# Kernel optimization log

Measured on AMD Instinct MI355X. Metric: run time of the kernel, lower is better.

The kernel has to match this reference:

```python
import jax, jax.numpy as jnp
import numpy as np

B, D, C = 4096, 4096, 1024


def setup_inputs() -> dict:
    key = jax.random.key(0)
    kx, kw = jax.random.split(key)
    x = jax.random.normal(kx, (B, D), dtype=jnp.float32)
    # kaiming_normal_ with nonlinearity='relu': std = sqrt(2 / fan_in)
    W = jax.random.normal(kw, (C, D), dtype=jnp.float32) * jnp.sqrt(2.0 / D)
    return {"x": x, "W": W}


def reference(x, W):
    # Original: -( (x[:, :, None] - W.T[None, :, :])**2 ).mean(axis=1)
    d = x.shape[1]
    x_sq = jnp.sum(x * x, axis=1, keepdims=True)        # [B, 1]
    w_sq = jnp.sum(W * W, axis=1)[None, :]              # [1, C]
    cross = jnp.einsum('bd,cd->bc', x, W)               # [B, C] tensor-core GEMM
    return -(x_sq - 2.0 * cross + w_sq) / d
```

## Files before the change

### kernel.cpp

```cpp
#include <hip/hip_runtime.h>
#include <hip/hip_bf16.h>


typedef float f32x4 __attribute__((ext_vector_type(4)));
typedef float f32x2 __attribute__((ext_vector_type(2)));
typedef float f32x16 __attribute__((ext_vector_type(16)));
typedef int i32x4 __attribute__((ext_vector_type(4)));
typedef int i32x8 __attribute__((ext_vector_type(8)));

#define BDIM 4096
#define DDIM 4096
#define CDIM 1024
#define TM 128
#define TN 128
#define BK 64
#define KSPLIT 4
#define NIT ((DDIM / KSPLIT) / BK)
#define SCALE 32.0f
#define INV_SS (1.0f/1024.0f)
#define PSCALE 0.0625f

#define SYNC_LGKM() asm volatile("s_waitcnt lgkmcnt(0)\n\ts_barrier" ::: "memory")

__global__ __launch_bounds__(256) void cvt_rowsq(
    const float* __restrict__ x, const float* __restrict__ W,
    unsigned char* __restrict__ xb, unsigned char* __restrict__ wb,
    float* __restrict__ xsq, float* __restrict__ wsq)
{
    const int lane = threadIdx.x & 63;
    const int row = blockIdx.x * 4 + (threadIdx.x >> 6);

    const float* src;
    unsigned char* dst;
    float* sq;
    if (row < BDIM) {
        src = x + (size_t)row * DDIM;
        dst = xb + (size_t)row * DDIM;
        sq = xsq + row;
    } else {
        int r = row - BDIM;
        src = W + (size_t)r * DDIM;
        dst = wb + (size_t)r * DDIM;
        sq = wsq + r;
    }

    const float4* s4 = (const float4*)src;
    unsigned int* d4 = (unsigned int*)dst;
    float a = 0.f;
    #pragma unroll
    for (int s = 0; s < DDIM / 4 / 64; ++s) {
        float4 f = s4[lane + 64 * s];
        a += f.x * f.x + f.y * f.y + f.z * f.z + f.w * f.w;
        unsigned int p = 0;
        p = __builtin_amdgcn_cvt_pk_fp8_f32(f.x * SCALE, f.y * SCALE, p, false);
        p = __builtin_amdgcn_cvt_pk_fp8_f32(f.z * SCALE, f.w * SCALE, p, true);
        d4[lane + 64 * s] = p;
    }
    #pragma unroll
    for (int off = 32; off > 0; off >>= 1) a += __shfl_down(a, off);
    if (lane == 0) *sq = a;
}

struct Pref { i32x4 a0, a1, b0, b1; };

__device__ __forceinline__ i32x8 rd8(const unsigned char* p0,
                                     const unsigned char* p1) {
    i32x4 lo = *(const i32x4*)p0;
    i32x4 hi = *(const i32x4*)p1;
    return __builtin_shufflevector(lo, hi, 0, 1, 2, 3, 4, 5, 6, 7);
}

#define MXMFMA(A, Bv, C)                                                  \
    __builtin_amdgcn_mfma_scale_f32_32x32x64_f8f6f4(                      \
        (A), (Bv), (C), 0, 0, 0, 0x7F7F7F7F, 0, 0x7F7F7F7F)

__global__ __launch_bounds__(256, 3) void gemm_eucl(
    const unsigned char* __restrict__ xb,
    const unsigned char* __restrict__ wb,
    unsigned int* __restrict__ part)
{
    __shared__ unsigned char sm[2 * 16384];

    const int tid = threadIdx.x;
    const int lane = tid & 63;
    const int wid = tid >> 6;
    const int bm = blockIdx.x * TM;
    const int bn = blockIdx.y * TN;
    const int ks = blockIdx.z * (DDIM / KSPLIT);
    const int wm = (wid >> 1) * 64;
    const int wn = (wid & 1) * 64;

    const int r0 = tid >> 2, c = tid & 3;
    const unsigned int oA0 = (unsigned int)((bm + r0) * DDIM + ks + c * 16);
    const unsigned int oA1 = oA0 + 64u * DDIM;
    const unsigned int oB0 = (unsigned int)((bn + r0) * DDIM + ks + c * 16);
    const unsigned int oB1 = oB0 + 64u * DDIM;

    const int wo0 = r0 * 64 + ((c ^ ((r0 >> 1) & 3)) * 16);

    const int sswz = (lane >> 1) & 3;
    const int c0 = (lane >> 5) * 2;
    const int m0 = wm + (lane & 31);
    const int n0 = wn + (lane & 31);
    const int aof0 = m0 * 64 + ((c0 ^ sswz) * 16);
    const int aof1 = m0 * 64 + (((c0 + 1) ^ sswz) * 16);
    const int bof0 = n0 * 64 + ((c0 ^ sswz) * 16);
    const int bof1 = n0 * 64 + (((c0 + 1) ^ sswz) * 16);

    f32x16 acc[4] = {};

#define LOADSET(S, KT)                                                   \
    do {                                                                 \
        (S).a0 = *(const i32x4*)(xb + oA0 + (KT) * BK);                  \
        (S).a1 = *(const i32x4*)(xb + oA1 + (KT) * BK);                  \
        (S).b0 = *(const i32x4*)(wb + oB0 + (KT) * BK);                  \
        (S).b1 = *(const i32x4*)(wb + oB1 + (KT) * BK);                  \
    } while (0)

#define WRITESET(buf, S)                                                 \
    do {                                                                 \
        unsigned char* sA = sm + (buf) * 16384;                          \
        unsigned char* sB = sA + 8192;                                   \
        *(i32x4*)(sA + wo0) = (S).a0;                                    \
        *(i32x4*)(sA + wo0 + 4096) = (S).a1;                             \
        *(i32x4*)(sB + wo0) = (S).b0;                                    \
        *(i32x4*)(sB + wo0 + 4096) = (S).b1;                             \
    } while (0)

#define COMPUTE(buf)                                                     \
    do {                                                                 \
        const unsigned char* sA = sm + (buf) * 16384;                    \
        const unsigned char* sB = sA + 8192;                             \
        i32x8 fb0 = rd8(sB + bof0, sB + bof1);                           \
        i32x8 fb1 = rd8(sB + bof0 + 2048, sB + bof1 + 2048);             \
        i32x8 fa0 = rd8(sA + aof0, sA + aof1);                           \
        acc[0] = MXMFMA(fa0, fb0, acc[0]);                               \
        i32x8 fa1 = rd8(sA + aof0 + 2048, sA + aof1 + 2048);             \
        acc[1] = MXMFMA(fa0, fb1, acc[1]);                               \
        acc[2] = MXMFMA(fa1, fb0, acc[2]);                               \
        acc[3] = MXMFMA(fa1, fb1, acc[3]);                               \
    } while (0)

    Pref S[3];
    LOADSET(S[0], 0);
    LOADSET(S[1], 1);
    LOADSET(S[2], 2);
    WRITESET(0, S[0]);
    SYNC_LGKM();

    #pragma unroll
    for (int k = 0; k < NIT - 1; ++k) {
        if (k < NIT - 3) LOADSET(S[k % 3], k + 3);
        COMPUTE(k & 1);
        WRITESET((k + 1) & 1, S[(k + 1) % 3]);
        SYNC_LGKM();
    }
    COMPUTE((NIT - 1) & 1);

    unsigned int* p = part
        + (((size_t)blockIdx.z * 256 + (blockIdx.x * 8 + blockIdx.y)) * 16) * 256;
    #pragma unroll
    for (int t = 0; t < 4; ++t)
        #pragma unroll
        for (int g = 0; g < 4; ++g) {
            unsigned int pk = 0;
            pk = __builtin_amdgcn_cvt_pk_fp8_f32(
                acc[t][g * 4 + 0] * PSCALE, acc[t][g * 4 + 1] * PSCALE, pk, false);
            pk = __builtin_amdgcn_cvt_pk_fp8_f32(
                acc[t][g * 4 + 2] * PSCALE, acc[t][g * 4 + 3] * PSCALE, pk, true);
            p[(t * 4 + g) * 256 + tid] = pk;
        }
#undef LOADSET
#undef WRITESET
#undef COMPUTE
}

__global__ __launch_bounds__(256) void reduce_out(
    const unsigned int* __restrict__ part, const float* __restrict__ xsq,
    const float* __restrict__ wsq, float* __restrict__ out)
{
    const int bid = blockIdx.x;
    const int bb = bid >> 1;
    const int f0 = (bid & 1) * 8;
    const int t = threadIdx.x;
    const int lane = t & 63;
    const int wid = t >> 6;
    const int bm = (bb >> 3) * TM, bn = (bb & 7) * TN;
    const int wm = (wid >> 1) * 64, wn = (wid & 1) * 64;
    const size_t sl = (size_t)256 * 16 * 256;
    const float c1 = 2.0f * 16.0f * INV_SS / (float)DDIM;
    const float c2 = 1.0f / (float)DDIM;

    #pragma unroll
    for (int f = f0; f < f0 + 8; ++f) {
        size_t o = ((size_t)bb * 16 + f) * 256 + t;
        f32x2 s01 = {0.f, 0.f}, s23 = {0.f, 0.f};
        #pragma unroll
        for (int z = 0; z < KSPLIT; ++z) {
            unsigned int u = part[o + (size_t)z * sl];
            s01 += __builtin_amdgcn_cvt_pk_f32_fp8(u, false);
            s23 += __builtin_amdgcn_cvt_pk_f32_fp8(u, true);
        }
        int t4 = f >> 2, g = f & 3;
        int it = t4 >> 1, jt = t4 & 1;
        int gn = bn + wn + jt * 32 + (lane & 31);
        float wv = wsq[gn];
        int gm0 = bm + wm + it * 32 + (lane >> 5) * 4 + g * 8;
        float sv[4] = {s01.x, s01.y, s23.x, s23.y};
        #pragma unroll
        for (int r = 0; r < 4; ++r) {
            out[(size_t)(gm0 + r) * CDIM + gn] = sv[r] * c1 - (xsq[gm0 + r] + wv) * c2;
        }
    }
}

__global__ void fallback_kernel(const float* __restrict__ x, const float* __restrict__ W,
                                float* __restrict__ out)
{
    int c = blockIdx.x * blockDim.x + threadIdx.x;
    int b = blockIdx.y;
    if (c >= CDIM) return;
    const float* xr = x + (size_t)b * DDIM;
    const float* wr = W + (size_t)c * DDIM;
    float xs = 0.f, ws = 0.f, cr = 0.f;
    for (int d = 0; d < DDIM; ++d) {
        float xv = xr[d], wv = wr[d];
        xs += xv * xv; ws += wv * wv; cr += xv * wv;
    }
    out[(size_t)b * CDIM + c] = (2.0f * cr - xs - ws) / (float)DDIM;
}

extern "C" void kernel_launch(void* const* d_in, const int* in_sizes, int n_in,
                              void* d_out, int out_size, void* d_ws, size_t ws_size,
                              hipStream_t stream) {
    const float* x = (const float*)d_in[0];
    const float* W = (const float*)d_in[1];
    float* out = (float*)d_out;

    size_t need = (size_t)(BDIM + CDIM) * DDIM
                + (size_t)(BDIM + CDIM) * sizeof(float)
                + (size_t)KSPLIT * BDIM * CDIM;
    if (ws_size < need) {
        fallback_kernel<<<dim3(CDIM / 256, BDIM), 256, 0, stream>>>(x, W, out);
        return;
    }

    unsigned char* xb = (unsigned char*)d_ws;
    unsigned char* wb = xb + (size_t)BDIM * DDIM;
    float* xsq = (float*)(wb + (size_t)CDIM * DDIM);
    float* wsq = xsq + BDIM;
    unsigned int* part = (unsigned int*)(wsq + CDIM);

    cvt_rowsq<<<(BDIM + CDIM) / 4, 256, 0, stream>>>(x, W, xb, wb, xsq, wsq);
    gemm_eucl<<<dim3(BDIM / TM, CDIM / TN, KSPLIT), 256, 0, stream>>>(xb, wb, part);
    reduce_out<<<512, 256, 0, stream>>>(part, xsq, wsq, out);
}
```

Measured before the change: 139.4 us.

## Load W fragments directly from global into registers, bypassing LDS

The B operand (W in fp8) is no longer staged through shared memory. Each lane now loads its MFMA fragment straight from global memory into registers and prefetches two iterations ahead. LDS traffic and footprint are halved, which may allow more blocks per CU. The cost is that each B row is read redundantly by the two waves that share it, through L1/L2, using more VGPRs and more global load instructions.

```diff
diff --git a/kernel.cpp b/kernel.cpp
--- a/kernel.cpp
+++ b/kernel.cpp
@@ -61,12 +61,10 @@
     if (lane == 0) *sq = a;
 }
 
-struct Pref { i32x4 a0, a1, b0, b1; };
-
-__device__ __forceinline__ i32x8 rd8(const unsigned char* p0,
-                                     const unsigned char* p1) {
-    i32x4 lo = *(const i32x4*)p0;
-    i32x4 hi = *(const i32x4*)p1;
+struct PrefA { i32x4 a0, a1; };
+struct PrefB { i32x4 b00, b01, b10, b11; };
+
+__device__ __forceinline__ i32x8 cat8(i32x4 lo, i32x4 hi) {
     return __builtin_shufflevector(lo, hi, 0, 1, 2, 3, 4, 5, 6, 7);
 }
 
@@ -79,7 +77,7 @@
     const unsigned char* __restrict__ wb,
     unsigned int* __restrict__ part)
 {
-    __shared__ unsigned char sm[2 * 16384];
+    __shared__ unsigned char sm[2 * 8192];
 
     const int tid = threadIdx.x;
     const int lane = tid & 63;
@@ -93,69 +91,74 @@
     const int r0 = tid >> 2, c = tid & 3;
     const unsigned int oA0 = (unsigned int)((bm + r0) * DDIM + ks + c * 16);
     const unsigned int oA1 = oA0 + 64u * DDIM;
-    const unsigned int oB0 = (unsigned int)((bn + r0) * DDIM + ks + c * 16);
-    const unsigned int oB1 = oB0 + 64u * DDIM;
 
     const int wo0 = r0 * 64 + ((c ^ ((r0 >> 1) & 3)) * 16);
 
     const int sswz = (lane >> 1) & 3;
     const int c0 = (lane >> 5) * 2;
     const int m0 = wm + (lane & 31);
-    const int n0 = wn + (lane & 31);
     const int aof0 = m0 * 64 + ((c0 ^ sswz) * 16);
     const int aof1 = m0 * 64 + (((c0 + 1) ^ sswz) * 16);
-    const int bof0 = n0 * 64 + ((c0 ^ sswz) * 16);
-    const int bof1 = n0 * 64 + (((c0 + 1) ^ sswz) * 16);
+
+    const unsigned char* pB0 =
+        wb + (size_t)(bn + wn + (lane & 31)) * DDIM + ks + (lane >> 5) * 32;
+    const unsigned char* pB1 = pB0 + (size_t)32 * DDIM;
 
     f32x16 acc[4] = {};
 
-#define LOADSET(S, KT)                                                   \
+#define ALOAD(S, KT)                                                     \
     do {                                                                 \
         (S).a0 = *(const i32x4*)(xb + oA0 + (KT) * BK);                  \
         (S).a1 = *(const i32x4*)(xb + oA1 + (KT) * BK);                  \
-        (S).b0 = *(const i32x4*)(wb + oB0 + (KT) * BK);                  \
-        (S).b1 = *(const i32x4*)(wb + oB1 + (KT) * BK);                  \
-    } while (0)
-
-#define WRITESET(buf, S)                                                 \
-    do {                                                                 \
-        unsigned char* sA = sm + (buf) * 16384;                          \
-        unsigned char* sB = sA + 8192;                                   \
+    } while (0)
+
+#define BLOAD(T, KT)                                                     \
+    do {                                                                 \
+        (T).b00 = *(const i32x4*)(pB0 + (KT) * BK);                      \
+        (T).b01 = *(const i32x4*)(pB0 + (KT) * BK + 16);                 \
+        (T).b10 = *(const i32x4*)(pB1 + (KT) * BK);                      \
+        (T).b11 = *(const i32x4*)(pB1 + (KT) * BK + 16);                 \
+    } while (0)
+
+#define AWRITE(buf, S)                                                   \
+    do {                                                                 \
+        unsigned char* sA = sm + (buf) * 8192;                           \
         *(i32x4*)(sA + wo0) = (S).a0;                                    \
         *(i32x4*)(sA + wo0 + 4096) = (S).a1;                             \
-        *(i32x4*)(sB + wo0) = (S).b0;                                    \
-        *(i32x4*)(sB + wo0 + 4096) = (S).b1;                             \
-    } while (0)
-
-#define COMPUTE(buf)                                                     \
-    do {                                                                 \
-        const unsigned char* sA = sm + (buf) * 16384;                    \
-        const unsigned char* sB = sA + 8192;                             \
-        i32x8 fb0 = rd8(sB + bof0, sB + bof1);                           \
-        i32x8 fb1 = rd8(sB + bof0 + 2048, sB + bof1 + 2048);             \
-        i32x8 fa0 = rd8(sA + aof0, sA + aof1);                           \
+    } while (0)
+
+#define COMPUTE(buf, T)                                                  \
+    do {                                                                 \
+        const unsigned char* sA = sm + (buf) * 8192;                     \
+        i32x8 fb0 = cat8((T).b00, (T).b01);                              \
+        i32x8 fb1 = cat8((T).b10, (T).b11);                              \
+        i32x8 fa0 = cat8(*(const i32x4*)(sA + aof0),                     \
+                         *(const i32x4*)(sA + aof1));                    \
         acc[0] = MXMFMA(fa0, fb0, acc[0]);                               \
-        i32x8 fa1 = rd8(sA + aof0 + 2048, sA + aof1 + 2048);             \
+        i32x8 fa1 = cat8(*(const i32x4*)(sA + aof0 + 2048),              \
+                         *(const i32x4*)(sA + aof1 + 2048));             \
         acc[1] = MXMFMA(fa0, fb1, acc[1]);                               \
         acc[2] = MXMFMA(fa1, fb0, acc[2]);                               \
         acc[3] = MXMFMA(fa1, fb1, acc[3]);                               \
     } while (0)
 
-    Pref S[3];
-    LOADSET(S[0], 0);
-    LOADSET(S[1], 1);
-    LOADSET(S[2], 2);
-    WRITESET(0, S[0]);
+    PrefA SA[3];
+    PrefB SB[3];
+    ALOAD(SA[0], 0); BLOAD(SB[0], 0);
+    ALOAD(SA[1], 1); BLOAD(SB[1], 1);
+    ALOAD(SA[2], 2);
+    AWRITE(0, SA[0]);
     SYNC_LGKM();
 
     #pragma unroll
     for (int k = 0; k < NIT - 1; ++k) {
-        if (k < NIT - 3) LOADSET(S[k % 3], k + 3);
-        COMPUTE(k & 1);
-        WRITESET((k + 1) & 1, S[(k + 1) % 3]);
+        if (k < NIT - 3) ALOAD(SA[k % 3], k + 3);
+        if (k < NIT - 2) BLOAD(SB[(k + 2) % 3], k + 2);
+        COMPUTE(k & 1, SB[k % 3]);
+        AWRITE((k + 1) & 1, SA[(k + 1) % 3]);
         SYNC_LGKM();
     }
-    COMPUTE((NIT - 1) & 1);
+    COMPUTE((NIT - 1) & 1, SB[(NIT - 1) % 3]);
 
     unsigned int* p = part
         + (((size_t)blockIdx.z * 256 + (blockIdx.x * 8 + blockIdx.y)) * 16) * 256;
@@ -170,8 +173,9 @@
                 acc[t][g * 4 + 2] * PSCALE, acc[t][g * 4 + 3] * PSCALE, pk, true);
             p[(t * 4 + g) * 256 + tid] = pk;
         }
-#undef LOADSET
-#undef WRITESET
+#undef ALOAD
+#undef BLOAD
+#undef AWRITE
 #undef COMPUTE
 }
 
```

Result: slower. 159.8 us (+14.6%).
